# Optimization experiments

Hardware: AMD Instinct MI355X
Metric: run time of the kernel (lower is better)

Reference implementation:

```python
import jax, jax.numpy as jnp
import numpy as np

N_NODES = 20000
N_EDGES = 640000
IN_DIM = 128
HID = 128
NUM_GRAPHS = 64


def setup_inputs() -> dict:
    key = jax.random.key(0)
    ks = jax.random.split(key, 12)
    x = jax.random.normal(ks[0], (N_NODES, IN_DIM), dtype=jnp.float32)
    edge_index = jax.random.randint(ks[1], (2, N_EDGES), 0, N_NODES, dtype=jnp.int64)
    batch = jnp.sort(jax.random.randint(ks[2], (N_NODES,), 0, NUM_GRAPHS, dtype=jnp.int64))
    edge_attr = jax.random.uniform(ks[3], (N_EDGES,), dtype=jnp.float32)
    s1 = 1.0 / np.sqrt(IN_DIM)
    s2 = 1.0 / np.sqrt(HID)
    # GraphConv layer 1: lin_rel (with bias) on aggregated messages, lin_root (no bias) on x
    W1_rel = jax.random.uniform(ks[4], (HID, IN_DIM), minval=-s1, maxval=s1, dtype=jnp.float32)
    b1 = jax.random.uniform(ks[5], (HID,), minval=-s1, maxval=s1, dtype=jnp.float32)
    W1_root = jax.random.uniform(ks[6], (HID, IN_DIM), minval=-s1, maxval=s1, dtype=jnp.float32)
    # GraphConv layer 3 (conv2 is unused in forward)
    W3_rel = jax.random.uniform(ks[7], (HID, HID), minval=-s2, maxval=s2, dtype=jnp.float32)
    b3 = jax.random.uniform(ks[8], (HID,), minval=-s2, maxval=s2, dtype=jnp.float32)
    W3_root = jax.random.uniform(ks[9], (HID, HID), minval=-s2, maxval=s2, dtype=jnp.float32)
    # Final linear head
    Wlin = jax.random.uniform(ks[10], (1, HID), minval=-s2, maxval=s2, dtype=jnp.float32)
    blin = jax.random.uniform(ks[11], (1,), minval=-s2, maxval=s2, dtype=jnp.float32)
    return {
        "x": x, "edge_index": edge_index, "batch": batch, "edge_attr": edge_attr,
        "W1_rel": W1_rel, "b1": b1, "W1_root": W1_root,
        "W3_rel": W3_rel, "b3": b3, "W3_root": W3_root,
        "Wlin": Wlin, "blin": blin, "num_graphs": NUM_GRAPHS,
    }


def graph_conv(x, src, dst, edge_w, W_rel, b_rel, W_root):
    # PyG GraphConv (aggr='add'): out = W_rel @ sum_{j in N(i)} w_ij * x_j + b_rel + W_root @ x_i
    msg = x[src] * edge_w[:, None]                       # [E, d] gather + scale
    agg = jax.ops.segment_sum(msg, dst, num_segments=x.shape[0])  # [N, d] scatter-add
    return agg @ W_rel.T + b_rel + x @ W_root.T


def reference(x, edge_index, batch, edge_attr,
              W1_rel, b1, W1_root, W3_rel, b3, W3_root, Wlin, blin, num_graphs):
    src, dst = edge_index[0], edge_index[1]
    h = graph_conv(x, src, dst, edge_attr, W1_rel, b1, W1_root)
    h = jax.nn.relu(h)
    # dropout p=0.5 is identity in eval mode
    h = graph_conv(h, src, dst, edge_attr, W3_rel, b3, W3_root)
    # global_mean_pool over per-node graph ids
    sums = jax.ops.segment_sum(h, batch, num_segments=num_graphs)          # [G, H]
    counts = jax.ops.segment_sum(jnp.ones((h.shape[0],), h.dtype), batch,
                                 num_segments=num_graphs)                  # [G]
    pooled = sums / jnp.maximum(counts, 1.0)[:, None]
    out = jax.nn.relu(pooled @ Wlin.T + blin)                              # [G, 1]
    return out
```

## Files before the change

### kernel.cpp

```cpp
#include <hip/hip_runtime.h>

#define N_NODES 20000
#define N_EDGES 640000
#define DIM 128
#define NGRAPH 64
#define NBUCK 313
#define CAP 2560
#define EPB 1024
#define NB_PART 625
#define NB_WCONV 32
#define NB_GEMM 1252
#define RED_BLOCKS 512

typedef __attribute__((ext_vector_type(8))) short short8;
typedef __attribute__((ext_vector_type(4))) float floatx4;

__device__ __forceinline__ unsigned int bf16rne(float f) {
    unsigned int u = __float_as_uint(f);
    return (u + 0x7FFFu + ((u >> 16) & 1u)) >> 16;
}

__device__ __forceinline__ int2 nt_load2(const int2* p) {
    long long v = __builtin_nontemporal_load((const long long*)p);
    int2 r;
    r.x = (int)(v & 0xFFFFFFFFll);
    r.y = (int)(v >> 32);
    return r;
}

__global__ __launch_bounds__(256) void k_part_prep(
    const int* __restrict__ src, const int* __restrict__ dst,
    const float* __restrict__ ew,
    const float* __restrict__ W1rel, const float* __restrict__ W1root,
    const float* __restrict__ W3rel, const float* __restrict__ W3root,
    const float* __restrict__ b3, const float* __restrict__ Wlin,
    int* __restrict__ gcursor, int2* __restrict__ part,
    unsigned short* __restrict__ wbh, unsigned short* __restrict__ wbl,
    float* __restrict__ vrel, float* __restrict__ vroot, float* __restrict__ cb3) {

    const int t = threadIdx.x;
    const int blk = blockIdx.x;

    if (blk < NB_PART) {
        __shared__ int lhist[NBUCK], lbase[NBUCK], gbase[NBUCK], lcur[NBUCK];
        __shared__ int2 lrec[EPB];
        for (int i = t; i < NBUCK; i += 256) lhist[i] = 0;
        __syncthreads();
        const int e0 = blk * EPB;
        const int tot = min(EPB, N_EDGES - e0);
        int mys[4], myd[4];
        float myw[4];
        for (int i = 0; i < 4; ++i) {
            int e = e0 + i * 256 + t;
            if (e < N_EDGES) {
                mys[i] = src[e];
                myd[i] = dst[e];
                myw[i] = ew[e];
                atomicAdd(&lhist[myd[i] >> 6], 1);
            } else {
                myd[i] = -1;
            }
        }
        __syncthreads();
        if (t < 64) {
            int carry = 0;
            for (int c = 0; c < 5; ++c) {
                int idx = c * 64 + t;
                int v = (idx < NBUCK) ? lhist[idx] : 0;
                int xv = v;
                for (int s = 1; s < 64; s <<= 1) {
                    int u = __shfl_up(xv, s);
                    if (t >= s) xv += u;
                }
                if (idx < NBUCK) { lbase[idx] = carry + xv - v; lcur[idx] = 0; }
                carry += __shfl(xv, 63);
            }
        }
        __syncthreads();
        for (int i = t; i < NBUCK; i += 256) {
            int cnt = lhist[i];
            gbase[i] = cnt ? (i * CAP + atomicAdd(&gcursor[i], cnt)) : 0;
        }
        __syncthreads();
        for (int i = 0; i < 4; ++i) {
            if (myd[i] >= 0) {
                int bb = myd[i] >> 6;
                int slot = lbase[bb] + atomicAdd(&lcur[bb], 1);
                lrec[slot] = make_int2((myd[i] << 16) | mys[i], __float_as_int(myw[i]));
            }
        }
        __syncthreads();
        for (int i = t; i < tot; i += 256) {
            int2 rc = lrec[i];
            int bb = ((unsigned)rc.x >> 16) >> 6;
            part[gbase[bb] + (i - lbase[bb])] = rc;
        }
    } else if (blk < NB_PART + NB_WCONV) {
        const int b = blk - NB_PART;
        for (int i = b * 256 + t; i < 256 * DIM; i += NB_WCONV * 256) {
            int n = i >> 7, k = i & 127;
            float v = (n < DIM) ? W1rel[n * DIM + k] : W1root[(n - DIM) * DIM + k];
            unsigned int h = bf16rne(v);
            wbh[i] = (unsigned short)h;
            wbl[i] = (unsigned short)bf16rne(v - __uint_as_float(h << 16));
        }
    } else {
        if (t < 64) {
            for (int kk = 0; kk < 2; ++kk) {
                int k = t + kk * 64;
                float sr = 0.f, so = 0.f;
                for (int h = 0; h < DIM; ++h) {
                    float wl = Wlin[h];
                    sr = fmaf(wl, W3rel[h * DIM + k], sr);
                    so = fmaf(wl, W3root[h * DIM + k], so);
                }
                vrel[k] = sr;
                vroot[k] = so;
            }
            float c = b3[t] * Wlin[t] + b3[t + 64] * Wlin[t + 64];
            for (int m = 32; m > 0; m >>= 1) c += __shfl_xor(c, m);
            if (t == 0) cb3[0] = c;
        }
    }
}

union SMem2 {
    struct { int2 lrec[CAP]; int nh[64], ncur[64]; } s;
    struct { unsigned short h[64 * DIM], l[64 * DIM]; } g;
};

__global__ __launch_bounds__(256) void k_sort_gemm(
    const int* __restrict__ gcursor, int2* __restrict__ part,
    int* __restrict__ off, int* __restrict__ nend,
    const float* __restrict__ x,
    const unsigned short* __restrict__ wbh, const unsigned short* __restrict__ wbl,
    const float* __restrict__ b1,
    unsigned short* __restrict__ yb, float* __restrict__ r) {
    __shared__ SMem2 sm;
    const int t = threadIdx.x;

    if (blockIdx.x < NBUCK) {
        const int b = blockIdx.x;
        const int base = b * CAP;
        const int cnt = min(gcursor[b], CAP);
        for (int i = t; i < cnt; i += 256) sm.s.lrec[i] = nt_load2(&part[base + i]);
        if (t < 64) sm.s.nh[t] = 0;
        __syncthreads();
        for (int i = t; i < cnt; i += 256)
            atomicAdd(&sm.s.nh[((unsigned)sm.s.lrec[i].x >> 16) & 63], 1);
        __syncthreads();
        if (t < 64) {
            int v = sm.s.nh[t];
            int xv = v;
            for (int s = 1; s < 64; s <<= 1) {
                int u = __shfl_up(xv, s);
                if (t >= s) xv += u;
            }
            int excl = xv - v;
            sm.s.ncur[t] = excl;
            int node = b * 64 + t;
            if (node < N_NODES) {
                off[node] = base + excl;
                nend[node] = base + excl + v;
            }
        }
        __syncthreads();
        for (int i = t; i < cnt; i += 256) {
            int2 rc = sm.s.lrec[i];
            int dl = ((unsigned)rc.x >> 16) & 63;
            int p = atomicAdd(&sm.s.ncur[dl], 1);
            part[base + p] = make_int2(rc.x & 0xFFFF, rc.y);
        }
    } else {
        const int tile = blockIdx.x - NBUCK;
        const int g = tile >> 2;
        const int col0 = (tile & 3) * 64;
        uint4* sh = (uint4*)sm.g.h;
        uint4* sl = (uint4*)sm.g.l;
        const uint4* gh = (const uint4*)wbh + (size_t)col0 * 16;
        const uint4* gl = (const uint4*)wbl + (size_t)col0 * 16;
        for (int i = t; i < 1024; i += 256) {
            int row = i >> 4, c = i & 15;
            int sc = row * 16 + (c ^ (row & 15));
            sh[sc] = gh[i];
            sl[sc] = gl[i];
        }
        __syncthreads();

        const int lane = t & 63;
        const int m = lane & 15;
        const int q = lane >> 4;
        const int row0 = g * 64 + (t >> 6) * 16;
        const int row = row0 + m;
        const bool ok = row < N_NODES;
        const short8* SH = (const short8*)sm.g.h;
        const short8* SL = (const short8*)sm.g.l;

        floatx4 acc[4];
        #pragma unroll
        for (int i = 0; i < 4; ++i) acc[i] = (floatx4)(0.f);

        #pragma unroll
        for (int kc = 0; kc < 4; ++kc) {
            float4 v0 = make_float4(0.f, 0.f, 0.f, 0.f);
            float4 v1 = make_float4(0.f, 0.f, 0.f, 0.f);
            if (ok) {
                const float4* xp = (const float4*)(x + (size_t)row * DIM + kc * 32 + q * 8);
                v0 = xp[0];
                v1 = xp[1];
            }
            float f[8] = {v0.x, v0.y, v0.z, v0.w, v1.x, v1.y, v1.z, v1.w};
            short8 ah, al;
            #pragma unroll
            for (int i = 0; i < 8; ++i) {
                unsigned int h = bf16rne(f[i]);
                ah[i] = (short)h;
                al[i] = (short)bf16rne(f[i] - __uint_as_float(h << 16));
            }
            #pragma unroll
            for (int nt = 0; nt < 4; ++nt) {
                int nl = nt * 16 + m;
                int cc = (kc * 4 + q) ^ m;
                short8 bh = SH[nl * 16 + cc];
                short8 bl = SL[nl * 16 + cc];
                acc[nt] = __builtin_amdgcn_mfma_f32_16x16x32_bf16(ah, bh, acc[nt], 0, 0, 0);
                acc[nt] = __builtin_amdgcn_mfma_f32_16x16x32_bf16(al, bh, acc[nt], 0, 0, 0);
                acc[nt] = __builtin_amdgcn_mfma_f32_16x16x32_bf16(ah, bl, acc[nt], 0, 0, 0);
            }
        }

        #pragma unroll
        for (int nt = 0; nt < 4; ++nt) {
            int col = col0 + nt * 16 + m;
            float bias = (col >= DIM) ? b1[col - DIM] : 0.f;
            #pragma unroll
            for (int reg = 0; reg < 4; ++reg) {
                int orow = row0 + q * 4 + reg;
                if (orow < N_NODES) {
                    float v = acc[nt][reg];
                    if (col < DIM)
                        yb[orow * DIM + col] = (unsigned short)bf16rne(v);
                    else
                        r[orow * DIM + (col - DIM)] = v + bias;
                }
            }
        }
    }
}

__global__ __launch_bounds__(256) void k_agg(const unsigned int* __restrict__ yb,
                                             const float2* __restrict__ r2,
                                             const int* __restrict__ off,
                                             const int* __restrict__ nend,
                                             const int2* __restrict__ grec,
                                             const float2* __restrict__ vrel2,
                                             const float2* __restrict__ vroot2,
                                             float* __restrict__ aout,
                                             float* __restrict__ bout) {
    const int lane = threadIdx.x & 63;
    const int node = blockIdx.x * 4 + (threadIdx.x >> 6);
    if (node >= N_NODES) return;

    const float2 rr = r2[(size_t)node * 64 + lane];
    const float2 vr = vrel2[lane];
    const float2 vo = vroot2[lane];

    int j = off[node];
    const int e1 = nend[node];
    float sx = 0.f, sy = 0.f;
    for (; j + 8 <= e1; j += 8) {
        int2 rc[8];
        #pragma unroll
        for (int u = 0; u < 8; ++u) rc[u] = nt_load2(&grec[j + u]);
        unsigned int v[8];
        #pragma unroll
        for (int u = 0; u < 8; ++u) v[u] = yb[rc[u].x * 64 + lane];
        #pragma unroll
        for (int u = 0; u < 8; ++u) {
            float w = __int_as_float(rc[u].y);
            sx = fmaf(w, __uint_as_float(v[u] << 16), sx);
            sy = fmaf(w, __uint_as_float(v[u] & 0xFFFF0000u), sy);
        }
    }
    for (; j < e1; ++j) {
        int2 rcs = nt_load2(&grec[j]);
        float w = __int_as_float(rcs.y);
        unsigned int vv = yb[rcs.x * 64 + lane];
        sx = fmaf(w, __uint_as_float(vv << 16), sx);
        sy = fmaf(w, __uint_as_float(vv & 0xFFFF0000u), sy);
    }
    float hx = fmaxf(sx + rr.x, 0.f);
    float hy = fmaxf(sy + rr.y, 0.f);
    float pa = hx * vr.x + hy * vr.y;
    float pb = hx * vo.x + hy * vo.y;
    for (int mm = 32; mm > 0; mm >>= 1) {
        pa += __shfl_xor(pa, mm);
        pb += __shfl_xor(pb, mm);
    }
    if (lane == 0) {
        aout[node] = pa;
        bout[node] = pb;
    }
}

__global__ __launch_bounds__(256) void k_reduce_final(
    const int2* __restrict__ grec, const int* __restrict__ off,
    const int* __restrict__ nend,
    const float* __restrict__ a, const float* __restrict__ bvec,
    const int* __restrict__ batch,
    float* __restrict__ gpart, int* __restrict__ gpartc,
    int* __restrict__ ticket_red,
    const float* __restrict__ cb3, const float* __restrict__ blin,
    float* __restrict__ out) {
    __shared__ float sbin[NGRAPH];
    __shared__ int cbin[NGRAPH];
    __shared__ int islast;
    const int t = threadIdx.x;
    for (int i = t; i < NGRAPH; i += 256) { sbin[i] = 0.f; cbin[i] = 0; }
    __syncthreads();
    const int lane = t & 63;
    const int gw = blockIdx.x * 4 + (t >> 6);
    const int nw = gridDim.x * 4;
    for (int node = gw; node < N_NODES; node += nw) {
        const int e0 = off[node], e1 = nend[node];
        const float bv = bvec[node];
        float s = 0.f;
        for (int j = e0 + lane; j < e1; j += 64) {
            int2 rc = nt_load2(&grec[j]);
            s = fmaf(__int_as_float(rc.y), a[rc.x], s);
        }
        for (int mm = 32; mm > 0; mm >>= 1) s += __shfl_xor(s, mm);
        if (lane == 0) {
            int g = batch[node];
            atomicAdd(&sbin[g], s + bv);
            atomicAdd(&cbin[g], 1);
        }
    }
    __syncthreads();
    const int slot = blockIdx.x & 63;
    for (int i = t; i < NGRAPH; i += 256) {
        atomicAdd(&gpart[slot * NGRAPH + i], sbin[i]);
        if (cbin[i]) atomicAdd(&gpartc[slot * NGRAPH + i], cbin[i]);
    }
    __syncthreads();
    if (t == 0) {
        __threadfence();
        islast = (atomicAdd(ticket_red, 1) == (int)gridDim.x - 1);
    }
    __syncthreads();
    if (islast) {
        __threadfence();
        if (t < NGRAPH) {
            float S = 0.f;
            int C = 0;
            for (int s2 = 0; s2 < 64; ++s2) {
                S += __hip_atomic_load(&gpart[s2 * NGRAPH + t], __ATOMIC_RELAXED,
                                       __HIP_MEMORY_SCOPE_AGENT);
                C += __hip_atomic_load(&gpartc[s2 * NGRAPH + t], __ATOMIC_RELAXED,
                                       __HIP_MEMORY_SCOPE_AGENT);
            }
            float denom = (C > 0) ? (float)C : 1.f;
            float v = (S + (float)C * cb3[0]) / denom + blin[0];
            out[t] = (v > 0.f) ? v : 0.f;
        }
    }
}

extern "C" void kernel_launch(void* const* d_in, const int* in_sizes, int n_in,
                              void* d_out, int out_size, void* d_ws, size_t ws_size,
                              hipStream_t stream) {
    const float* x = (const float*)d_in[0];
    const int* edge_index = (const int*)d_in[1];
    const int* src = edge_index;
    const int* dst = edge_index + N_EDGES;
    const int* batch = (const int*)d_in[2];
    const float* ew = (const float*)d_in[3];
    const float* W1rel = (const float*)d_in[4];
    const float* b1 = (const float*)d_in[5];
    const float* W1root = (const float*)d_in[6];
    const float* W3rel = (const float*)d_in[7];
    const float* b3 = (const float*)d_in[8];
    const float* W3root = (const float*)d_in[9];
    const float* Wlin = (const float*)d_in[10];
    const float* blin = (const float*)d_in[11];
    float* out = (float*)d_out;

    char* w = (char*)d_ws;
    size_t o = 0;
    auto alloc = [&](size_t bytes) -> void* {
        void* p = w + o;
        o += bytes;
        o = (o + 255) & ~(size_t)255;
        return p;
    };
    char* zbase = (char*)alloc((NBUCK + 1) * 4 + 64 * NGRAPH * 4 * 2);
    int* gcursor = (int*)zbase;
    int* ticket_red = gcursor + NBUCK;
    float* gpart = (float*)(zbase + (NBUCK + 1) * 4);
    int* gpartc = (int*)(zbase + (NBUCK + 1) * 4 + 64 * NGRAPH * 4);
    const size_t zbytes = (NBUCK + 1) * 4 + 64 * NGRAPH * 4 * 2;

    unsigned short* wbh = (unsigned short*)alloc((size_t)256 * DIM * 2);
    unsigned short* wbl = (unsigned short*)alloc((size_t)256 * DIM * 2);
    unsigned short* yb = (unsigned short*)alloc((size_t)N_NODES * DIM * 2);
    float* r = (float*)alloc((size_t)N_NODES * DIM * 4);
    int2* part = (int2*)alloc((size_t)NBUCK * CAP * 8);
    int* off = (int*)alloc((size_t)N_NODES * 4);
    int* nend = (int*)alloc((size_t)N_NODES * 4);
    float* a = (float*)alloc((size_t)N_NODES * 4);
    float* b = (float*)alloc((size_t)N_NODES * 4);
    float* vrel = (float*)alloc(DIM * 4);
    float* vroot = (float*)alloc(DIM * 4);
    float* cb3 = (float*)alloc(4);

    hipMemsetAsync(zbase, 0, zbytes, stream);

    k_part_prep<<<NB_PART + NB_WCONV + 1, 256, 0, stream>>>(
        src, dst, ew, W1rel, W1root, W3rel, W3root, b3, Wlin,
        gcursor, part, wbh, wbl, vrel, vroot, cb3);

    k_sort_gemm<<<NBUCK + NB_GEMM, 256, 0, stream>>>(
        gcursor, part, off, nend, x, wbh, wbl, b1, yb, r);

    k_agg<<<(N_NODES + 3) / 4, 256, 0, stream>>>(
        (const unsigned int*)yb, (const float2*)r, off, nend, part,
        (const float2*)vrel, (const float2*)vroot, a, b);

    k_reduce_final<<<RED_BLOCKS, 256, 0, stream>>>(
        part, off, nend, a, b, batch, gpart, gpartc, ticket_red, cb3, blin, out);
}
```

Measured before the change: 180.1 us.

## Fuse weight bf16 split into GEMM blocks and reschedule partition/GEMM/sort kernels

Removes the separate weight-conversion blocks: each GEMM block now reads the fp32 W1 weights and does the hi/lo bf16 split in-register while filling shared memory. The GEMM now runs alongside the edge partitioning in one launch, and the per-bucket sort moves to its own small kernel. Part of the reduction-buffer zeroing shifts from the memset into the prep block. This trades a dependency stage for redundant per-block weight conversion and a new standalone sort launch.

```diff
diff --git a/kernel.cpp b/kernel.cpp
--- a/kernel.cpp
+++ b/kernel.cpp
@@ -8,7 +8,6 @@
 #define CAP 2560
 #define EPB 1024
 #define NB_PART 625
-#define NB_WCONV 32
 #define NB_GEMM 1252
 #define RED_BLOCKS 512
 
@@ -28,23 +27,29 @@
     return r;
 }
 
-__global__ __launch_bounds__(256) void k_part_prep(
+union SMem1 {
+    struct { int lhist[NBUCK], lbase[NBUCK], gbase[NBUCK], lcur[NBUCK]; int2 lrec[EPB]; } p;
+    struct { unsigned short h[64 * DIM], l[64 * DIM]; } g;
+};
+
+__global__ __launch_bounds__(256) void k_part_gemm(
     const int* __restrict__ src, const int* __restrict__ dst,
-    const float* __restrict__ ew,
+    const float* __restrict__ ew, const float* __restrict__ x,
     const float* __restrict__ W1rel, const float* __restrict__ W1root,
+    const float* __restrict__ b1,
     const float* __restrict__ W3rel, const float* __restrict__ W3root,
     const float* __restrict__ b3, const float* __restrict__ Wlin,
     int* __restrict__ gcursor, int2* __restrict__ part,
-    unsigned short* __restrict__ wbh, unsigned short* __restrict__ wbl,
-    float* __restrict__ vrel, float* __restrict__ vroot, float* __restrict__ cb3) {
-
+    unsigned short* __restrict__ yb, float* __restrict__ r,
+    float* __restrict__ vrel, float* __restrict__ vroot, float* __restrict__ cb3,
+    int* __restrict__ zwords ) {
+
+    __shared__ SMem1 sm;
     const int t = threadIdx.x;
     const int blk = blockIdx.x;
 
     if (blk < NB_PART) {
-        __shared__ int lhist[NBUCK], lbase[NBUCK], gbase[NBUCK], lcur[NBUCK];
-        __shared__ int2 lrec[EPB];
-        for (int i = t; i < NBUCK; i += 256) lhist[i] = 0;
+        for (int i = t; i < NBUCK; i += 256) sm.p.lhist[i] = 0;
         __syncthreads();
         const int e0 = blk * EPB;
         const int tot = min(EPB, N_EDGES - e0);
@@ -56,7 +61,7 @@
                 mys[i] = src[e];
                 myd[i] = dst[e];
                 myw[i] = ew[e];
-                atomicAdd(&lhist[myd[i] >> 6], 1);
+                atomicAdd(&sm.p.lhist[myd[i] >> 6], 1);
             } else {
                 myd[i] = -1;
             }
@@ -66,124 +71,64 @@
             int carry = 0;
             for (int c = 0; c < 5; ++c) {
                 int idx = c * 64 + t;
-                int v = (idx < NBUCK) ? lhist[idx] : 0;
+                int v = (idx < NBUCK) ? sm.p.lhist[idx] : 0;
                 int xv = v;
                 for (int s = 1; s < 64; s <<= 1) {
                     int u = __shfl_up(xv, s);
                     if (t >= s) xv += u;
                 }
-                if (idx < NBUCK) { lbase[idx] = carry + xv - v; lcur[idx] = 0; }
+                if (idx < NBUCK) { sm.p.lbase[idx] = carry + xv - v; sm.p.lcur[idx] = 0; }
                 carry += __shfl(xv, 63);
             }
         }
         __syncthreads();
         for (int i = t; i < NBUCK; i += 256) {
-            int cnt = lhist[i];
-            gbase[i] = cnt ? (i * CAP + atomicAdd(&gcursor[i], cnt)) : 0;
+            int cnt = sm.p.lhist[i];
+            sm.p.gbase[i] = cnt ? (i * CAP + atomicAdd(&gcursor[i], cnt)) : 0;
         }
         __syncthreads();
         for (int i = 0; i < 4; ++i) {
             if (myd[i] >= 0) {
                 int bb = myd[i] >> 6;
-                int slot = lbase[bb] + atomicAdd(&lcur[bb], 1);
-                lrec[slot] = make_int2((myd[i] << 16) | mys[i], __float_as_int(myw[i]));
+                int slot = sm.p.lbase[bb] + atomicAdd(&sm.p.lcur[bb], 1);
+                sm.p.lrec[slot] = make_int2((myd[i] << 16) | mys[i], __float_as_int(myw[i]));
             }
         }
         __syncthreads();
         for (int i = t; i < tot; i += 256) {
-            int2 rc = lrec[i];
+            int2 rc = sm.p.lrec[i];
             int bb = ((unsigned)rc.x >> 16) >> 6;
-            part[gbase[bb] + (i - lbase[bb])] = rc;
-        }
-    } else if (blk < NB_PART + NB_WCONV) {
-        const int b = blk - NB_PART;
-        for (int i = b * 256 + t; i < 256 * DIM; i += NB_WCONV * 256) {
-            int n = i >> 7, k = i & 127;
-            float v = (n < DIM) ? W1rel[n * DIM + k] : W1root[(n - DIM) * DIM + k];
-            unsigned int h = bf16rne(v);
-            wbh[i] = (unsigned short)h;
-            wbl[i] = (unsigned short)bf16rne(v - __uint_as_float(h << 16));
-        }
-    } else {
-        if (t < 64) {
-            for (int kk = 0; kk < 2; ++kk) {
-                int k = t + kk * 64;
-                float sr = 0.f, so = 0.f;
-                for (int h = 0; h < DIM; ++h) {
-                    float wl = Wlin[h];
-                    sr = fmaf(wl, W3rel[h * DIM + k], sr);
-                    so = fmaf(wl, W3root[h * DIM + k], so);
-                }
-                vrel[k] = sr;
-                vroot[k] = so;
-            }
-            float c = b3[t] * Wlin[t] + b3[t + 64] * Wlin[t + 64];
-            for (int m = 32; m > 0; m >>= 1) c += __shfl_xor(c, m);
-            if (t == 0) cb3[0] = c;
-        }
-    }
-}
-
-union SMem2 {
-    struct { int2 lrec[CAP]; int nh[64], ncur[64]; } s;
-    struct { unsigned short h[64 * DIM], l[64 * DIM]; } g;
-};
-
-__global__ __launch_bounds__(256) void k_sort_gemm(
-    const int* __restrict__ gcursor, int2* __restrict__ part,
-    int* __restrict__ off, int* __restrict__ nend,
-    const float* __restrict__ x,
-    const unsigned short* __restrict__ wbh, const unsigned short* __restrict__ wbl,
-    const float* __restrict__ b1,
-    unsigned short* __restrict__ yb, float* __restrict__ r) {
-    __shared__ SMem2 sm;
-    const int t = threadIdx.x;
-
-    if (blockIdx.x < NBUCK) {
-        const int b = blockIdx.x;
-        const int base = b * CAP;
-        const int cnt = min(gcursor[b], CAP);
-        for (int i = t; i < cnt; i += 256) sm.s.lrec[i] = nt_load2(&part[base + i]);
-        if (t < 64) sm.s.nh[t] = 0;
-        __syncthreads();
-        for (int i = t; i < cnt; i += 256)
-            atomicAdd(&sm.s.nh[((unsigned)sm.s.lrec[i].x >> 16) & 63], 1);
-        __syncthreads();
-        if (t < 64) {
-            int v = sm.s.nh[t];
-            int xv = v;
-            for (int s = 1; s < 64; s <<= 1) {
-                int u = __shfl_up(xv, s);
-                if (t >= s) xv += u;
-            }
-            int excl = xv - v;
-            sm.s.ncur[t] = excl;
-            int node = b * 64 + t;
-            if (node < N_NODES) {
-                off[node] = base + excl;
-                nend[node] = base + excl + v;
-            }
-        }
-        __syncthreads();
-        for (int i = t; i < cnt; i += 256) {
-            int2 rc = sm.s.lrec[i];
-            int dl = ((unsigned)rc.x >> 16) & 63;
-            int p = atomicAdd(&sm.s.ncur[dl], 1);
-            part[base + p] = make_int2(rc.x & 0xFFFF, rc.y);
-        }
-    } else {
-        const int tile = blockIdx.x - NBUCK;
+            part[sm.p.gbase[bb] + (i - sm.p.lbase[bb])] = rc;
+        }
+    } else if (blk < NB_PART + NB_GEMM) {
+        const int tile = blk - NB_PART;
         const int g = tile >> 2;
         const int col0 = (tile & 3) * 64;
+
         uint4* sh = (uint4*)sm.g.h;
         uint4* sl = (uint4*)sm.g.l;
-        const uint4* gh = (const uint4*)wbh + (size_t)col0 * 16;
-        const uint4* gl = (const uint4*)wbl + (size_t)col0 * 16;
         for (int i = t; i < 1024; i += 256) {
             int row = i >> 4, c = i & 15;
+            int wrow = col0 + row;
+            const float* srcw = (wrow < DIM) ? (W1rel + (size_t)wrow * DIM)
+                                             : (W1root + (size_t)(wrow - DIM) * DIM);
+            float4 f0 = ((const float4*)srcw)[c * 2];
+            float4 f1 = ((const float4*)srcw)[c * 2 + 1];
+            float f[8] = {f0.x, f0.y, f0.z, f0.w, f1.x, f1.y, f1.z, f1.w};
+            unsigned int hh[8], ll[8];
+            #pragma unroll
+            for (int u = 0; u < 8; ++u) {
+                hh[u] = bf16rne(f[u]);
+                ll[u] = bf16rne(f[u] - __uint_as_float(hh[u] << 16));
+            }
+            uint4 ph, pl;
+            ph.x = hh[0] | (hh[1] << 16); ph.y = hh[2] | (hh[3] << 16);
+            ph.z = hh[4] | (hh[5] << 16); ph.w = hh[6] | (hh[7] << 16);
+            pl.x = ll[0] | (ll[1] << 16); pl.y = ll[2] | (ll[3] << 16);
+            pl.z = ll[4] | (ll[5] << 16); pl.w = ll[6] | (ll[7] << 16);
             int sc = row * 16 + (c ^ (row & 15));
-            sh[sc] = gh[i];
-            sl[sc] = gl[i];
+            sh[sc] = ph;
+            sl[sc] = pl;
         }
         __syncthreads();
 
@@ -245,6 +190,63 @@
                 }
             }
         }
+    } else {
+        if (t < 64) {
+            for (int kk = 0; kk < 2; ++kk) {
+                int k = t + kk * 64;
+                float sr = 0.f, so = 0.f;
+                for (int h = 0; h < DIM; ++h) {
+                    float wl = Wlin[h];
+                    sr = fmaf(wl, W3rel[h * DIM + k], sr);
+                    so = fmaf(wl, W3root[h * DIM + k], so);
+                }
+                vrel[k] = sr;
+                vroot[k] = so;
+            }
+            float c = b3[t] * Wlin[t] + b3[t + 64] * Wlin[t + 64];
+            for (int m = 32; m > 0; m >>= 1) c += __shfl_xor(c, m);
+            if (t == 0) cb3[0] = c;
+        }
+        for (int i = t; i < 64 * NGRAPH * 2 + 1; i += 256) zwords[i] = 0;
+    }
+}
+
+__global__ __launch_bounds__(256) void k_sort(
+    const int* __restrict__ gcursor, int2* __restrict__ part,
+    int* __restrict__ off, int* __restrict__ nend) {
+    __shared__ int2 lrec[CAP];
+    __shared__ int nh[64], ncur[64];
+    const int t = threadIdx.x;
+    const int b = blockIdx.x;
+    const int base = b * CAP;
+    const int cnt = min(gcursor[b], CAP);
+    for (int i = t; i < cnt; i += 256) lrec[i] = nt_load2(&part[base + i]);
+    if (t < 64) nh[t] = 0;
+    __syncthreads();
+    for (int i = t; i < cnt; i += 256)
+        atomicAdd(&nh[((unsigned)lrec[i].x >> 16) & 63], 1);
+    __syncthreads();
+    if (t < 64) {
+        int v = nh[t];
+        int xv = v;
+        for (int s = 1; s < 64; s <<= 1) {
+            int u = __shfl_up(xv, s);
+            if (t >= s) xv += u;
+        }
+        int excl = xv - v;
+        ncur[t] = excl;
+        int node = b * 64 + t;
+        if (node < N_NODES) {
+            off[node] = base + excl;
+            nend[node] = base + excl + v;
+        }
+    }
+    __syncthreads();
+    for (int i = t; i < cnt; i += 256) {
+        int2 rc = lrec[i];
+        int dl = ((unsigned)rc.x >> 16) & 63;
+        int p = atomicAdd(&ncur[dl], 1);
+        part[base + p] = make_int2(rc.x & 0xFFFF, rc.y);
     }
 }
 
@@ -393,15 +395,12 @@
         o = (o + 255) & ~(size_t)255;
         return p;
     };
-    char* zbase = (char*)alloc((NBUCK + 1) * 4 + 64 * NGRAPH * 4 * 2);
-    int* gcursor = (int*)zbase;
-    int* ticket_red = gcursor + NBUCK;
-    float* gpart = (float*)(zbase + (NBUCK + 1) * 4);
-    int* gpartc = (int*)(zbase + (NBUCK + 1) * 4 + 64 * NGRAPH * 4);
-    const size_t zbytes = (NBUCK + 1) * 4 + 64 * NGRAPH * 4 * 2;
-
-    unsigned short* wbh = (unsigned short*)alloc((size_t)256 * DIM * 2);
-    unsigned short* wbl = (unsigned short*)alloc((size_t)256 * DIM * 2);
+    int* gcursor = (int*)alloc(NBUCK * 4);
+    int* zwords = (int*)alloc((64 * NGRAPH * 2 + 1) * 4);
+    float* gpart = (float*)zwords;
+    int* gpartc = zwords + 64 * NGRAPH;
+    int* ticket_red = zwords + 64 * NGRAPH * 2;
+
     unsigned short* yb = (unsigned short*)alloc((size_t)N_NODES * DIM * 2);
     float* r = (float*)alloc((size_t)N_NODES * DIM * 4);
     int2* part = (int2*)alloc((size_t)NBUCK * CAP * 8);
@@ -413,14 +412,13 @@
     float* vroot = (float*)alloc(DIM * 4);
     float* cb3 = (float*)alloc(4);
 
-    hipMemsetAsync(zbase, 0, zbytes, stream);
-
-    k_part_prep<<<NB_PART + NB_WCONV + 1, 256, 0, stream>>>(
-        src, dst, ew, W1rel, W1root, W3rel, W3root, b3, Wlin,
-        gcursor, part, wbh, wbl, vrel, vroot, cb3);
-
-    k_sort_gemm<<<NBUCK + NB_GEMM, 256, 0, stream>>>(
-        gcursor, part, off, nend, x, wbh, wbl, b1, yb, r);
+    hipMemsetAsync(gcursor, 0, NBUCK * 4, stream);
+
+    k_part_gemm<<<NB_PART + NB_GEMM + 1, 256, 0, stream>>>(
+        src, dst, ew, x, W1rel, W1root, b1, W3rel, W3root, b3, Wlin,
+        gcursor, part, yb, r, vrel, vroot, cb3, zwords);
+
+    k_sort<<<NBUCK, 256, 0, stream>>>(gcursor, part, off, nend);
 
     k_agg<<<(N_NODES + 3) / 4, 256, 0, stream>>>(
         (const unsigned int*)yb, (const float2*)r, off, nend, part,
```

Result: no change. 182.9 us (+1.6%).
